# Kernel tuning notes

Hardware: AMD Instinct MI355X
Metric: run time of the kernel (lower is better)

## Reference

```python
import jax, jax.numpy as jnp
import numpy as np

BS, N_CH, H, R, N_AGGR, T = 32768, 16, 128, 64, 4, 128


def _xavier(key, shape):
    fan_in, fan_out = shape[-2], shape[-1]
    lim = float(np.sqrt(6.0 / (fan_in + fan_out)))
    return jax.random.uniform(key, shape, jnp.float32, -lim, lim)


def setup_inputs() -> dict:
    key = jax.random.key(0)
    ks = jax.random.split(key, 9)
    return {
        "neighbour_h": jax.random.normal(ks[0], (BS, N_CH, H), jnp.float32),
        "type_embs": jax.random.normal(ks[1], (BS, T), jnp.float32),
        "A": _xavier(ks[2], (N_AGGR, H, R)),
        "B": _xavier(ks[3], (N_AGGR, R, R)),
        "A_b": _xavier(ks[4], (N_AGGR, 1, R)),
        "U_type": _xavier(ks[5], (N_AGGR, T, R)),
        "b_type": _xavier(ks[6], (N_AGGR, 1, R)),
        "U_output": _xavier(ks[7], (N_AGGR, R, H)),
        "b_output": _xavier(ks[8], (N_AGGR, 1, H)),
    }


def reference(neighbour_h, type_embs, A, B, A_b, U_type, b_type, U_output, b_output):
    bs = neighbour_h.shape[0]
    # per-child input projection: (bs, n_ch, n_aggr, rank)
    ris = jnp.einsum('bch,ahr->bcar', neighbour_h, A) + A_b[:, 0]
    # initial state from node-type embedding: (bs, n_aggr, rank)
    r0 = jnp.einsum('bt,atr->bar', type_embs, U_type) + b_type[:, 0]
    # linear recurrence over children: r_t = r_{t-1} @ B + a_t
    a_seq = jnp.moveaxis(ris, 1, 0)  # (n_ch, bs, n_aggr, rank)

    def step(r, a_t):
        return jnp.einsum('bar,arq->baq', r, B) + a_t, None

    r_fin, _ = jax.lax.scan(step, r0, a_seq)
    # output projection: (bs, n_aggr, h_size)
    out = jnp.einsum('bar,arh->bah', r_fin, U_output) + b_output[:, 0]
    return out.reshape(bs, -1)
```

## Files before the change

kernel.cpp:

```cpp
#include <hip/hip_runtime.h>
#include <hip/hip_bf16.h>


typedef short bf16x8 __attribute__((ext_vector_type(8)));
typedef float f32x4  __attribute__((ext_vector_type(4)));

__device__ __forceinline__ unsigned f2bfbits(float f) {
    unsigned u = __builtin_bit_cast(unsigned, f);
    return (u + 0x7FFFu + ((u >> 16) & 1u)) >> 16;
}
__device__ __forceinline__ unsigned pack2(float a, float b) {
    unsigned lo = (unsigned)__builtin_bit_cast(unsigned short, __float2bfloat16(a));
    unsigned hi = (unsigned)__builtin_bit_cast(unsigned short, __float2bfloat16(b));
    return lo | (hi << 16);
}

#define FS 68

__global__ __launch_bounds__(512) void tt_prep(
    const float* __restrict__ nh,
    const float* __restrict__ te,
    const float* __restrict__ Ag,
    const float* __restrict__ Bg,
    const float* __restrict__ Abg,
    const float* __restrict__ Utg,
    const float* __restrict__ btg,
    const float* __restrict__ Uog,
    const float* __restrict__ bog,
    unsigned short* __restrict__ Bp,
    float* __restrict__ biasOut,
    unsigned short* __restrict__ Ap)
{
    __shared__ __align__(16) float L[23552];
    const int t = threadIdx.x;
    const int bid = blockIdx.x;

    if (bid >= 72) {
        const int cb = bid - 72;
        const int mt = cb >> 3;
        const int r = t >> 2, q = t & 3;
        for (int kt = cb & 7; kt < 34; kt += 8) {
            const float* src = (kt < 32)
                ? nh + ((size_t)(mt * 128 + r) * 2048 + kt * 64 + q * 16)
                : te + ((size_t)(mt * 128 + r) * 128 + (kt - 32) * 64 + q * 16);
            float4 v0 = ((const float4*)src)[0];
            float4 v1 = ((const float4*)src)[1];
            float4 v2 = ((const float4*)src)[2];
            float4 v3 = ((const float4*)src)[3];
            uint4 w0, w1;
            w0.x = pack2(v0.x, v0.y);  w0.y = pack2(v0.z, v0.w);
            w0.z = pack2(v1.x, v1.y);  w0.w = pack2(v1.z, v1.w);
            w1.x = pack2(v2.x, v2.y);  w1.y = pack2(v2.z, v2.w);
            w1.z = pack2(v3.x, v3.y);  w1.w = pack2(v3.z, v3.w);
            unsigned short* dst = Ap + (size_t)(mt * 34 + kt) * 8192;
            *(uint4*)(dst + (2 * q)     * 1024 + r * 8) = w0;
            *(uint4*)(dst + (2 * q + 1) * 1024 + r * 8) = w1;
        }
        return;
    }

    auto mm = [&](float* d, const float* x, const float* y, const float* add) {
        const int r = t >> 3, c0 = (t & 7) << 3;
        float acc[8];
#pragma unroll
        for (int j = 0; j < 8; ++j) acc[j] = 0.f;
        for (int k = 0; k < 64; ++k) {
            const float a = x[r * FS + k];
            const float4 y0 = *(const float4*)(y + k * FS + c0);
            const float4 y1 = *(const float4*)(y + k * FS + c0 + 4);
            acc[0] += a * y0.x; acc[1] += a * y0.y;
            acc[2] += a * y0.z; acc[3] += a * y0.w;
            acc[4] += a * y1.x; acc[5] += a * y1.y;
            acc[6] += a * y1.z; acc[7] += a * y1.w;
        }
        if (add) {
#pragma unroll
            for (int j = 0; j < 8; ++j) acc[j] += add[r * FS + c0 + j];
        }
#pragma unroll
        for (int j = 0; j < 8; ++j) d[r * FS + c0 + j] = acc[j];
    };

    float* buf[4];
    buf[0] = L;
    buf[1] = L + 4352;
    buf[2] = L + 8704;
    buf[3] = L + 13056;
    float* const Pbuf = L + 17408;
    float* const UC   = L + 21504;

    if (bid < 68) {
        int a, p, kbase;
        const float* src;
        if (bid < 64) { a = bid >> 4; const int c = bid & 15; p = 15 - c; kbase = c * 128; src = Ag  + a * 8192; }
        else          { a = bid - 64; p = 16; kbase = 2048;               src = Utg + a * 8192; }
        const float* Bmat = Bg + a * 4096;

        for (int i = t; i < 4096; i += 512) {
            const int row = i >> 6, col = i & 63;
            buf[0][row * FS + col] = Bmat[i];
            buf[2][row * FS + col] = (row == col) ? 1.f : 0.f;
        }
        __syncthreads();
        int bcur = 0, rcur = 2;
        int e = p;
        while (e) {
            if (e & 1) { mm(buf[rcur ^ 1], buf[rcur], buf[bcur], nullptr); rcur ^= 1; __syncthreads(); }
            e >>= 1;
            if (e)     { mm(buf[bcur ^ 1], buf[bcur], buf[bcur], nullptr); bcur ^= 1; __syncthreads(); }
        }

        {
            const int prow = t >> 3, pc0 = (t & 7) << 3;
#pragma unroll
            for (int j = 0; j < 8; ++j)
                Pbuf[prow * 64 + pc0 + j] = buf[rcur][prow * FS + pc0 + j];
        }
        __syncthreads();

        float* M1 = L;
        {
            const int i = t >> 2, r0 = (t & 3) << 4;
            float acc[16];
#pragma unroll
            for (int j = 0; j < 16; ++j) acc[j] = 0.f;
            for (int q = 0; q < 64; ++q) {
                const float av = src[i * 64 + q];
                const float4* pr = (const float4*)(Pbuf + q * 64 + r0);
#pragma unroll
                for (int jj = 0; jj < 4; ++jj) {
                    float4 v = pr[jj];
                    acc[4 * jj + 0] += av * v.x;
                    acc[4 * jj + 1] += av * v.y;
                    acc[4 * jj + 2] += av * v.z;
                    acc[4 * jj + 3] += av * v.w;
                }
            }
#pragma unroll
            for (int j = 0; j < 16; ++j) M1[i * 65 + r0 + j] = acc[j];
        }
        __syncthreads();

        const float* UoA = Uog + a * 8192;
        const int i = t >> 2, h0 = (t & 3) << 5;
        float acc2[32];
#pragma unroll
        for (int j = 0; j < 32; ++j) acc2[j] = 0.f;
        for (int ch = 0; ch < 4; ++ch) {
            __syncthreads();
            for (int idx = t; idx < 2048; idx += 512) UC[idx] = UoA[ch * 2048 + idx];
            __syncthreads();
            for (int rr = 0; rr < 16; ++rr) {
                const float m = M1[i * 65 + ch * 16 + rr];
                const float4* ur = (const float4*)(UC + rr * 128 + h0);
#pragma unroll
                for (int jj = 0; jj < 8; ++jj) {
                    float4 v = ur[jj];
                    acc2[4 * jj + 0] += m * v.x;
                    acc2[4 * jj + 1] += m * v.y;
                    acc2[4 * jj + 2] += m * v.z;
                    acc2[4 * jj + 3] += m * v.w;
                }
            }
        }
        {
            const int k = kbase + i;
            const int kt = k >> 6, slot = (k >> 3) & 7, widx = k & 7;
#pragma unroll
            for (int j = 0; j < 32; ++j) {
                const int n = a * 128 + h0 + j;
                Bp[((size_t)(((n >> 7) * 34 + kt) * 8 + slot)) * 1024 + (n & 127) * 8 + widx] =
                    (unsigned short)f2bfbits(acc2[j]);
            }
        }
    } else {
        const int a = bid - 68;
        const float* Bmat = Bg + a * 4096;
        for (int i = t; i < 4096; i += 512) {
            const int row = i >> 6, col = i & 63;
            buf[0][row * FS + col] = Bmat[i];
            buf[2][row * FS + col] = (row == col) ? 1.f : 0.f;
        }
        __syncthreads();
        int bcur = 0, scur = 2;
        for (int rnd = 0; rnd < 4; ++rnd) {
            mm(buf[scur ^ 1], buf[bcur], buf[scur], buf[scur]);
            mm(buf[bcur ^ 1], buf[bcur], buf[bcur], nullptr);
            __syncthreads();
            scur ^= 1; bcur ^= 1;
        }
        float* vv = Pbuf;
        if (t < 64) {
            float acc = 0.f;
            const float* S16 = buf[scur];
            const float* B16 = buf[bcur];
            for (int q = 0; q < 64; ++q)
                acc += Abg[a * 64 + q] * S16[q * FS + t]
                     + btg[a * 64 + q] * B16[q * FS + t];
            vv[t] = acc;
        }
        __syncthreads();
        if (t < 128) {
            float accb = bog[a * 128 + t];
            const float* UoA = Uog + a * 8192;
            for (int r = 0; r < 64; ++r) accb += vv[r] * UoA[r * 128 + t];
            biasOut[a * 128 + t] = accb;
        }
    }
}
#undef FS

#define WAITBAR(NSTR) \
    asm volatile("s_waitcnt vmcnt(" NSTR ")\n\ts_barrier" ::: "memory")

__global__ __launch_bounds__(256) void tt_gemm(
    const unsigned short* __restrict__ Ap,
    const unsigned short* __restrict__ Bp,
    const float* __restrict__ bias,
    float* __restrict__ out)
{
    __shared__ __align__(16) char Lds[49152];

    const int t = threadIdx.x;
    const int lane = t & 63, w = t >> 6;
    const int lt = (blockIdx.x & 7) * 128 + (blockIdx.x >> 3);
    const int mt = lt >> 2, nb = lt & 3;
    const int wr = w >> 1, wc = w & 1;
    const int lx = lane & 15, lg = lane >> 4;

    const char* const asrc = (const char*)Ap + (size_t)mt * 557056 + w * 2048 + lane * 16;
    const char* const bsrc = (const char*)Bp + (size_t)nb * 557056 + w * 2048 + lane * 16;

    const int aro = lg * 2048 + (wr * 64 + lx) * 16;
    const int bro = lg * 2048 + (wc * 64 + lx) * 16;

    f32x4 acc[4][4] = {};

#define STAGE(slot_, s_) do {                                                  \
    const char* _ga = asrc + (size_t)(s_) * 8192;                              \
    const char* _gb = bsrc + (size_t)(s_) * 8192;                              \
    char* _ld = Lds + (slot_) * 16384 + w * 2048;                              \
    _Pragma("unroll")                                                          \
    for (int _j = 0; _j < 2; ++_j)                                             \
        __builtin_amdgcn_global_load_lds(                                      \
            (const __attribute__((address_space(1))) unsigned int*)(_ga + _j * 1024), \
            (__attribute__((address_space(3))) unsigned int*)(_ld + _j * 1024),\
            16, 0, 0);                                                         \
    _Pragma("unroll")                                                          \
    for (int _j = 0; _j < 2; ++_j)                                             \
        __builtin_amdgcn_global_load_lds(                                      \
            (const __attribute__((address_space(1))) unsigned int*)(_gb + _j * 1024), \
            (__attribute__((address_space(3))) unsigned int*)(_ld + 8192 + _j * 1024), \
            16, 0, 0);                                                         \
} while (0)

    STAGE(0, 0);
    STAGE(1, 1);
    WAITBAR("4");

    int cur = 0;
#pragma unroll 1
    for (int s = 0; s < 68; ++s) {
        const int nxt2 = (cur >= 1) ? cur - 1 : cur + 2;
        if (s + 2 < 68) STAGE(nxt2, s + 2);

        const char* Ab = Lds + cur * 16384;
        bf16x8 aF[4], bF[4];
#pragma unroll
        for (int f = 0; f < 4; ++f) {
            aF[f] = *(const bf16x8*)(Ab + aro + f * 256);
            bF[f] = *(const bf16x8*)(Ab + 8192 + bro + f * 256);
        }
#pragma unroll
        for (int fm = 0; fm < 4; ++fm)
#pragma unroll
            for (int fn = 0; fn < 4; ++fn)
                acc[fm][fn] = __builtin_amdgcn_mfma_f32_16x16x32_bf16(
                    aF[fm], bF[fn], acc[fm][fn], 0, 0, 0);

        if (s + 2 < 68)      WAITBAR("4");
        else if (s + 1 < 68) WAITBAR("0");
        cur = (cur == 2) ? 0 : cur + 1;
    }
#undef STAGE

    const int orow = mt * 128 + wr * 64 + lg * 4;
    const int ocol = nb * 128 + wc * 64 + lx;
    float bv[4];
#pragma unroll
    for (int fn = 0; fn < 4; ++fn) bv[fn] = bias[ocol + fn * 16];
#pragma unroll
    for (int fm = 0; fm < 4; ++fm)
#pragma unroll
        for (int fn = 0; fn < 4; ++fn)
#pragma unroll
            for (int j = 0; j < 4; ++j)
                out[(size_t)(orow + fm * 16 + j) * 512 + ocol + fn * 16] =
                    acc[fm][fn][j] + bv[fn];
}

#define SYNC_NODRAIN() do {                                   \
    asm volatile("s_waitcnt lgkmcnt(0)" ::: "memory");        \
    __builtin_amdgcn_s_barrier();                             \
} while (0)

__global__ __launch_bounds__(256) void tt_gemm_fb(
    const float* __restrict__ nh,
    const float* __restrict__ te,
    const unsigned short* __restrict__ Bp,
    const float* __restrict__ bias,
    float* __restrict__ out)
{
    __shared__ __align__(16) char Ab[16384];

    const int t = threadIdx.x;
    const int lane = t & 63, wave = t >> 6;
    const int lt = (blockIdx.x & 7) * 128 + (blockIdx.x >> 3);
    const int m0 = (lt >> 1) * 64;
    const int wc = (lt & 1) * 4 + wave;
    const int lx = lane & 15, lg = lane >> 4;

    const int r = t >> 2, c = t & 3;
    const float* nhp = nh + (size_t)(m0 + r) * 2048 + c * 16;
    const float* tep = te + (size_t)(m0 + r) * 128  + c * 16;
    const int awoff = (c >> 1) * 4096 + (c & 1) * 2048 + r * 16;
    const int aroff = lg * 1024 + lx * 16;

    const char* const wbase = (const char*)Bp + (size_t)(wc >> 1) * 557056
                              + ((wc & 1) * 64 + lx) * 16 + lg * 2048;

    f32x4 acc[4][4] = {};
    float4 va0[4], va1[4];
    uint4  bF0[4][2], bF1[4][2];

#define LOADA(dst, kt_) do {                                                   \
    const float* _p = ((kt_) < 32) ? (nhp + (kt_) * 64) : (tep + ((kt_) - 32) * 64); \
    _Pragma("unroll")                                                          \
    for (int _j = 0; _j < 4; ++_j) dst[_j] = *(const float4*)(_p + 4 * _j);    \
} while (0)

#define WRITEA(src, d_) do {                                                   \
    uint4 _w0, _w1;                                                            \
    _w0.x = pack2(src[0].x, src[0].y);  _w0.y = pack2(src[0].z, src[0].w);     \
    _w0.z = pack2(src[1].x, src[1].y);  _w0.w = pack2(src[1].z, src[1].w);     \
    _w1.x = pack2(src[2].x, src[2].y);  _w1.y = pack2(src[2].z, src[2].w);     \
    _w1.z = pack2(src[3].x, src[3].y);  _w1.w = pack2(src[3].z, src[3].w);     \
    *(uint4*)(Ab + (d_) * 8192 + awoff)        = _w0;                          \
    *(uint4*)(Ab + (d_) * 8192 + awoff + 1024) = _w1;                          \
} while (0)

#define LOADB(dst, kt_) do {                                                   \
    const char* _q = wbase + (size_t)(kt_) * 16384;                            \
    _Pragma("unroll")                                                          \
    for (int _kk = 0; _kk < 2; ++_kk)                                          \
        _Pragma("unroll")                                                      \
        for (int _fn = 0; _fn < 4; ++_fn)                                      \
            dst[_fn][_kk] = *(const uint4*)(_q + _kk * 8192 + _fn * 256);      \
} while (0)

#define COMPUTE(d_, bsrc) do {                                                 \
    _Pragma("unroll")                                                          \
    for (int _kk = 0; _kk < 2; ++_kk) {                                        \
        bf16x8 _aF[4];                                                         \
        _Pragma("unroll")                                                      \
        for (int _fm = 0; _fm < 4; ++_fm)                                      \
            _aF[_fm] = *(const bf16x8*)(Ab + (d_) * 8192 + _kk * 4096 + aroff + _fm * 256); \
        _Pragma("unroll")                                                      \
        for (int _fm = 0; _fm < 4; ++_fm)                                      \
            _Pragma("unroll")                                                  \
            for (int _fn = 0; _fn < 4; ++_fn)                                  \
                acc[_fm][_fn] = __builtin_amdgcn_mfma_f32_16x16x32_bf16(       \
                    _aF[_fm], __builtin_bit_cast(bf16x8, bsrc[_fn][_kk]),      \
                    acc[_fm][_fn], 0, 0, 0);                                   \
    }                                                                          \
} while (0)

    LOADA(va0, 0);
    WRITEA(va0, 0);
    LOADA(va1, 1);
    LOADA(va0, 2);
    LOADB(bF0, 0);
    LOADB(bF1, 1);
    SYNC_NODRAIN();

#pragma unroll 1
    for (int kt = 0; kt < 34; kt += 2) {
        WRITEA(va1, 1);
        if (kt + 3 < 34) LOADA(va1, kt + 3);
        COMPUTE(0, bF0);
        if (kt + 2 < 34) LOADB(bF0, kt + 2);
        SYNC_NODRAIN();

        if (kt + 2 < 34) {
            WRITEA(va0, 0);
            if (kt + 4 < 34) LOADA(va0, kt + 4);
        }
        COMPUTE(1, bF1);
        if (kt + 3 < 34) LOADB(bF1, kt + 3);
        SYNC_NODRAIN();
    }
#undef LOADA
#undef WRITEA
#undef LOADB
#undef COMPUTE

    const int orow = m0 + lg * 4;
    const int ocol = wc * 64 + lx;
    float bv[4];
#pragma unroll
    for (int fn = 0; fn < 4; ++fn) bv[fn] = bias[ocol + fn * 16];
#pragma unroll
    for (int fm = 0; fm < 4; ++fm)
#pragma unroll
        for (int fn = 0; fn < 4; ++fn)
#pragma unroll
            for (int j = 0; j < 4; ++j)
                out[(size_t)(orow + fm * 16 + j) * 512 + ocol + fn * 16] =
                    acc[fm][fn][j] + bv[fn];
}

extern "C" void kernel_launch(void* const* d_in, const int* in_sizes, int n_in,
                              void* d_out, int out_size, void* d_ws, size_t ws_size,
                              hipStream_t stream) {
    const float* nh  = (const float*)d_in[0];
    const float* te  = (const float*)d_in[1];
    const float* Ag  = (const float*)d_in[2];
    const float* Bg  = (const float*)d_in[3];
    const float* Abg = (const float*)d_in[4];
    const float* Utg = (const float*)d_in[5];
    const float* btg = (const float*)d_in[6];
    const float* Uog = (const float*)d_in[7];
    const float* bog = (const float*)d_in[8];

    unsigned short* Bp = (unsigned short*)d_ws;
    float* bias = (float*)((char*)d_ws + 2228224);
    unsigned short* Ap = (unsigned short*)((char*)d_ws + 2230272);
    float* out = (float*)d_out;

    const bool fast = ws_size >= (size_t)144836608;

    if (fast) {
        hipLaunchKernelGGL(tt_prep, dim3(72 + 2048), dim3(512), 0, stream,
                           nh, te, Ag, Bg, Abg, Utg, btg, Uog, bog, Bp, bias, Ap);
        hipLaunchKernelGGL(tt_gemm, dim3(1024), dim3(256), 0, stream,
                           Ap, Bp, bias, out);
    } else {
        hipLaunchKernelGGL(tt_prep, dim3(72), dim3(512), 0, stream,
                           nh, te, Ag, Bg, Abg, Utg, btg, Uog, bog, Bp, bias, Ap);
        hipLaunchKernelGGL(tt_gemm_fb, dim3(1024), dim3(256), 0, stream,
                           nh, te, Bp, bias, out);
    }
}
```

Baseline: 196.0 us.

## Enlarge GEMM tiles to 256x256 with 8 waves and interleaved staged pipeline

Rewrites the bf16 MFMA GEMM to use 256x256 output tiles per 512-thread block, with each wave computing a 128x64 sub-tile. The K loop now moves 64-wide K-tiles through double-buffered 128KB LDS, and global-to-LDS loads are interleaved between quarter-blocks of MFMAs. Barriers and s_setprio are placed to keep the matrix units busy. The intent is more operand reuse and less global/LDS traffic per flop. The trade-offs are a grid of only 256 blocks, heavy LDS use that allows one block per CU, and many more barriers.

```diff
diff --git a/kernel.cpp b/kernel.cpp
--- a/kernel.cpp
+++ b/kernel.cpp
@@ -210,87 +210,181 @@
 }
 #undef FS
 
-#define WAITBAR(NSTR) \
-    asm volatile("s_waitcnt vmcnt(" NSTR ")\n\ts_barrier" ::: "memory")
-
-__global__ __launch_bounds__(256) void tt_gemm(
+__global__ __launch_bounds__(512) void tt_gemm(
     const unsigned short* __restrict__ Ap,
     const unsigned short* __restrict__ Bp,
     const float* __restrict__ bias,
     float* __restrict__ out)
 {
-    __shared__ __align__(16) char Lds[49152];
+    __shared__ __align__(16) char Lds[131072];
 
     const int t = threadIdx.x;
     const int lane = t & 63, w = t >> 6;
-    const int lt = (blockIdx.x & 7) * 128 + (blockIdx.x >> 3);
-    const int mt = lt >> 2, nb = lt & 3;
-    const int wr = w >> 1, wc = w & 1;
+    const int lt = (blockIdx.x & 7) * 32 + (blockIdx.x >> 3);
+    const int m0 = (lt >> 1) * 256;
+    const int nblk = lt & 1;
+    const int wr = w >> 2, wc = w & 3;
     const int lx = lane & 15, lg = lane >> 4;
 
-    const char* const asrc = (const char*)Ap + (size_t)mt * 557056 + w * 2048 + lane * 16;
-    const char* const bsrc = (const char*)Bp + (size_t)nb * 557056 + w * 2048 + lane * 16;
-
-    const int aro = lg * 2048 + (wr * 64 + lx) * 16;
-    const int bro = lg * 2048 + (wc * 64 + lx) * 16;
-
-    f32x4 acc[4][4] = {};
-
-#define STAGE(slot_, s_) do {                                                  \
-    const char* _ga = asrc + (size_t)(s_) * 8192;                              \
-    const char* _gb = bsrc + (size_t)(s_) * 8192;                              \
-    char* _ld = Lds + (slot_) * 16384 + w * 2048;                              \
+    const char* const apb = (const char*)Ap + (size_t)(m0 >> 7) * 34 * 16384
+                            + w * 1024 + lane * 16;
+    const char* const bpb = (const char*)Bp + (size_t)(nblk * 2) * 34 * 16384
+                            + w * 1024 + lane * 16;
+    char* const La = Lds;
+    char* const Lb = Lds + 65536;
+
+    const int aro = wr * 16384 + lx * 16;
+    int bco[4];
+#pragma unroll
+    for (int fn = 0; fn < 4; ++fn) {
+        const int col = wc * 64 + fn * 16 + lx;
+        bco[fn] = (col >> 7) * 16384 + (col & 127) * 16;
+    }
+
+    f32x4 acc[8][4] = {};
+    bf16x8 aF0[4][2], aF1[4][2], bF0[2][2], bF1[2][2];
+
+#define BAR()  __builtin_amdgcn_s_barrier()
+#define LGKM0() do { asm volatile("s_waitcnt lgkmcnt(0)" ::: "memory"); \
+                     __builtin_amdgcn_sched_barrier(0); } while (0)
+#define PRIO(x) __builtin_amdgcn_s_setprio(x)
+#define VM(NSTR) asm volatile("s_waitcnt vmcnt(" NSTR ")" ::: "memory")
+
+#define STAGEA(d_, h_, kt_) do {                                               \
+    const char* _s = apb + (size_t)((h_) * 34 + (kt_)) * 16384;                \
+    char* _d = La + (d_) * 32768 + (h_) * 16384 + w * 1024;                    \
+    __builtin_amdgcn_global_load_lds(                                          \
+        (const __attribute__((address_space(1))) unsigned int*)_s,             \
+        (__attribute__((address_space(3))) unsigned int*)_d, 16, 0, 0);        \
+    __builtin_amdgcn_global_load_lds(                                          \
+        (const __attribute__((address_space(1))) unsigned int*)(_s + 8192),    \
+        (__attribute__((address_space(3))) unsigned int*)(_d + 8192), 16, 0, 0); \
+} while (0)
+
+#define STAGEB(d_, h_, kt_) do {                                               \
+    const char* _s = bpb + (size_t)((h_) * 34 + (kt_)) * 16384;                \
+    char* _d = Lb + (d_) * 32768 + (h_) * 16384 + w * 1024;                    \
+    __builtin_amdgcn_global_load_lds(                                          \
+        (const __attribute__((address_space(1))) unsigned int*)_s,             \
+        (__attribute__((address_space(3))) unsigned int*)_d, 16, 0, 0);        \
+    __builtin_amdgcn_global_load_lds(                                          \
+        (const __attribute__((address_space(1))) unsigned int*)(_s + 8192),    \
+        (__attribute__((address_space(3))) unsigned int*)(_d + 8192), 16, 0, 0); \
+} while (0)
+
+#define RDA(dst, d_, fmb) do {                                                 \
     _Pragma("unroll")                                                          \
-    for (int _j = 0; _j < 2; ++_j)                                             \
-        __builtin_amdgcn_global_load_lds(                                      \
-            (const __attribute__((address_space(1))) unsigned int*)(_ga + _j * 1024), \
-            (__attribute__((address_space(3))) unsigned int*)(_ld + _j * 1024),\
-            16, 0, 0);                                                         \
+    for (int _f = 0; _f < 4; ++_f)                                             \
+        _Pragma("unroll")                                                      \
+        for (int _k = 0; _k < 2; ++_k)                                         \
+            dst[_f][_k] = *(const bf16x8*)(La + (d_) * 32768 +                 \
+                (_k * 4 + lg) * 2048 + aro + ((fmb) + _f) * 256);              \
+} while (0)
+
+#define RDB(dst, d_, fnb) do {                                                 \
     _Pragma("unroll")                                                          \
-    for (int _j = 0; _j < 2; ++_j)                                             \
-        __builtin_amdgcn_global_load_lds(                                      \
-            (const __attribute__((address_space(1))) unsigned int*)(_gb + _j * 1024), \
-            (__attribute__((address_space(3))) unsigned int*)(_ld + 8192 + _j * 1024), \
-            16, 0, 0);                                                         \
-} while (0)
-
-    STAGE(0, 0);
-    STAGE(1, 1);
-    WAITBAR("4");
-
-    int cur = 0;
+    for (int _f = 0; _f < 2; ++_f)                                             \
+        _Pragma("unroll")                                                      \
+        for (int _k = 0; _k < 2; ++_k)                                         \
+            dst[_f][_k] = *(const bf16x8*)(Lb + (d_) * 32768 +                 \
+                (_k * 4 + lg) * 2048 + bco[(fnb) + _f]);                       \
+} while (0)
+
+#define QMFMA(fmb, fnb, af, bf) do {                                           \
+    _Pragma("unroll")                                                          \
+    for (int _f = 0; _f < 4; ++_f)                                             \
+        _Pragma("unroll")                                                      \
+        for (int _n = 0; _n < 2; ++_n)                                         \
+            _Pragma("unroll")                                                  \
+            for (int _k = 0; _k < 2; ++_k)                                     \
+                acc[(fmb) + _f][(fnb) + _n] =                                  \
+                    __builtin_amdgcn_mfma_f32_16x16x32_bf16(                   \
+                        af[_f][_k], bf[_n][_k],                                \
+                        acc[(fmb) + _f][(fnb) + _n], 0, 0, 0);                 \
+} while (0)
+
+    STAGEA(0, 0, 0); STAGEA(0, 1, 0);
+    STAGEB(0, 0, 0); STAGEB(0, 1, 0);
+    STAGEA(1, 0, 1);
+    asm volatile("s_waitcnt vmcnt(0)" ::: "memory");
+    BAR();
+
 #pragma unroll 1
-    for (int s = 0; s < 68; ++s) {
-        const int nxt2 = (cur >= 1) ? cur - 1 : cur + 2;
-        if (s + 2 < 68) STAGE(nxt2, s + 2);
-
-        const char* Ab = Lds + cur * 16384;
-        bf16x8 aF[4], bF[4];
-#pragma unroll
-        for (int f = 0; f < 4; ++f) {
-            aF[f] = *(const bf16x8*)(Ab + aro + f * 256);
-            bF[f] = *(const bf16x8*)(Ab + 8192 + bro + f * 256);
-        }
-#pragma unroll
-        for (int fm = 0; fm < 4; ++fm)
-#pragma unroll
-            for (int fn = 0; fn < 4; ++fn)
-                acc[fm][fn] = __builtin_amdgcn_mfma_f32_16x16x32_bf16(
-                    aF[fm], bF[fn], acc[fm][fn], 0, 0, 0);
-
-        if (s + 2 < 68)      WAITBAR("4");
-        else if (s + 1 < 68) WAITBAR("0");
-        cur = (cur == 2) ? 0 : cur + 1;
+    for (int i = 0; i < 17; ++i) {
+        const int t1 = 2 * i + 1;
+        const int ta = 2 * i + 2, tb = 2 * i + 3;
+        const bool ga = ta < 34, gb = tb < 34;
+
+        STAGEA(1, 1, t1);
+        RDA(aF0, 0, 0);
+        RDB(bF0, 0, 0);
+        BAR(); LGKM0(); PRIO(1);
+        QMFMA(0, 0, aF0, bF0);
+        PRIO(0); BAR();
+
+        STAGEB(1, 0, t1);
+        RDB(bF1, 0, 2);
+        BAR(); LGKM0(); PRIO(1);
+        QMFMA(0, 2, aF0, bF1);
+        PRIO(0); BAR();
+
+        STAGEB(1, 1, t1);
+        RDA(aF1, 0, 4);
+        BAR(); LGKM0(); PRIO(1);
+        QMFMA(4, 0, aF1, bF0);
+        PRIO(0); BAR();
+
+        if (ga) STAGEA(0, 0, ta);
+        BAR(); PRIO(1);
+        QMFMA(4, 2, aF1, bF1);
+        PRIO(0);
+        if (ga) VM("2"); else VM("0");
+        BAR();
+
+        if (ga) STAGEA(0, 1, ta);
+        RDA(aF0, 1, 0);
+        RDB(bF0, 1, 0);
+        BAR(); LGKM0(); PRIO(1);
+        QMFMA(0, 0, aF0, bF0);
+        PRIO(0); BAR();
+
+        if (ga) STAGEB(0, 0, ta);
+        RDB(bF1, 1, 2);
+        BAR(); LGKM0(); PRIO(1);
+        QMFMA(0, 2, aF0, bF1);
+        PRIO(0); BAR();
+
+        if (ga) STAGEB(0, 1, ta);
+        RDA(aF1, 1, 4);
+        BAR(); LGKM0(); PRIO(1);
+        QMFMA(4, 0, aF1, bF0);
+        PRIO(0); BAR();
+
+        if (gb) STAGEA(1, 0, tb);
+        BAR(); PRIO(1);
+        QMFMA(4, 2, aF1, bF1);
+        PRIO(0);
+        if (gb) VM("2"); else VM("0");
+        BAR();
     }
-#undef STAGE
-
-    const int orow = mt * 128 + wr * 64 + lg * 4;
-    const int ocol = nb * 128 + wc * 64 + lx;
+
+#undef QMFMA
+#undef RDB
+#undef RDA
+#undef STAGEB
+#undef STAGEA
+#undef VM
+#undef PRIO
+#undef LGKM0
+#undef BAR
+
+    const int orow = m0 + wr * 128 + lg * 4;
+    const int ocol = nblk * 256 + wc * 64 + lx;
     float bv[4];
 #pragma unroll
     for (int fn = 0; fn < 4; ++fn) bv[fn] = bias[ocol + fn * 16];
 #pragma unroll
-    for (int fm = 0; fm < 4; ++fm)
+    for (int fm = 0; fm < 8; ++fm)
 #pragma unroll
         for (int fn = 0; fn < 4; ++fn)
 #pragma unroll
@@ -442,7 +536,7 @@
     if (fast) {
         hipLaunchKernelGGL(tt_prep, dim3(72 + 2048), dim3(512), 0, stream,
                            nh, te, Ag, Bg, Abg, Utg, btg, Uog, bog, Bp, bias, Ap);
-        hipLaunchKernelGGL(tt_gemm, dim3(1024), dim3(256), 0, stream,
+        hipLaunchKernelGGL(tt_gemm, dim3(256), dim3(512), 0, stream,
                            Ap, Bp, bias, out);
     } else {
         hipLaunchKernelGGL(tt_prep, dim3(72), dim3(512), 0, stream,
```

Result: faster. 165.3 us, median of 2 (-15.6%).
